# Kernel tuning notes

Measured on AMD Instinct MI355X. Metric: run time of the kernel, lower is better.

## Reference

```python
import jax, jax.numpy as jnp
import numpy as np

N, E = 50000, 800000          # nodes, edges
DC, EC, H, L = 128, 16, 64, 3 # data/edge channels, hidden, num GENConv layers
EPS_MSG = 1e-7                # GENConv message eps
LN_EPS = 1e-5                 # torch LayerNorm eps


def setup_inputs() -> dict:
    key = jax.random.key(0)
    ks = jax.random.split(key, 8)
    s = 0.05
    return {
        "x": jax.random.normal(ks[0], (N, DC), jnp.float32),
        "edge_index": jax.random.randint(ks[1], (2, E), 0, N),
        "edge_attr": jax.random.normal(ks[2], (E, EC), jnp.float32),
        # encoders
        "node_W": jax.random.normal(ks[3], (DC, H), jnp.float32) * s,
        "node_b": jnp.zeros((H,), jnp.float32),
        "edge_W": jax.random.normal(ks[4], (EC, H), jnp.float32) * s,
        "edge_b": jnp.zeros((H,), jnp.float32),
        # per-layer GENConv params (stacked over L layers)
        "t": jnp.ones((L,), jnp.float32),                       # learnable softmax temperature
        "mlp1_W": jax.random.normal(ks[5], (L, H, 2 * H), jnp.float32) * s,
        "mlp1_b": jnp.zeros((L, 2 * H), jnp.float32),
        "mlp_ln_g": jnp.ones((L, 2 * H), jnp.float32),
        "mlp_ln_b": jnp.zeros((L, 2 * H), jnp.float32),
        "mlp2_W": jax.random.normal(ks[6], (L, 2 * H, H), jnp.float32) * s,
        "mlp2_b": jnp.zeros((L, H), jnp.float32),
        # DeepGCNLayer res+ pre-norm params (index 0 also used as the final norm)
        "blk_ln_g": jnp.ones((L, H), jnp.float32),
        "blk_ln_b": jnp.zeros((L, H), jnp.float32),
    }


def _layernorm(h, g, b):
    mu = jnp.mean(h, axis=-1, keepdims=True)
    var = jnp.var(h, axis=-1, keepdims=True)
    return (h - mu) * jax.lax.rsqrt(var + LN_EPS) * g + b


def _genconv(h, src, dst, eattr, t, W1, b1, lng, lnb, W2, b2):
    # message: relu(x_j + edge_attr) + eps   -> [E, H]
    msg = jax.nn.relu(h[src] + eattr) + EPS_MSG
    # softmax aggregation over incoming edges of each dst node (per feature)
    s = msg * t
    smax = jax.ops.segment_max(s, dst, num_segments=N)
    e = jnp.exp(s - smax[dst])
    denom = jax.ops.segment_sum(e, dst, num_segments=N)
    w = e / denom[dst]
    agg = jax.ops.segment_sum(msg * w, dst, num_segments=N)
    out = agg + h  # root (x_r) residual inside GENConv
    # MLP: Linear(H,2H) -> LayerNorm -> ReLU -> Linear(2H,H)
    y = jax.nn.relu(_layernorm(out @ W1 + b1, lng, lnb))
    return y @ W2 + b2


def reference(x, edge_index, edge_attr, node_W, node_b, edge_W, edge_b, t,
              mlp1_W, mlp1_b, mlp_ln_g, mlp_ln_b, mlp2_W, mlp2_b,
              blk_ln_g, blk_ln_b):
    src, dst = edge_index[0], edge_index[1]
    h = x @ node_W + node_b
    ea = edge_attr @ edge_W + edge_b
    # layer 0: conv only (no pre-norm), as in DeeperGCN.forward
    h = _genconv(h, src, dst, ea, t[0], mlp1_W[0], mlp1_b[0],
                 mlp_ln_g[0], mlp_ln_b[0], mlp2_W[0], mlp2_b[0])
    # layers 1..L-1: res+ blocks (norm -> relu -> conv -> residual); dropout=0 in eval
    for i in range(1, L):
        z = jax.nn.relu(_layernorm(h, blk_ln_g[i], blk_ln_b[i]))
        h = h + _genconv(z, src, dst, ea, t[i], mlp1_W[i], mlp1_b[i],
                         mlp_ln_g[i], mlp_ln_b[i], mlp2_W[i], mlp2_b[i])
    # final: layers[0].norm + relu (dropout identity in eval)
    return jax.nn.relu(_layernorm(h, blk_ln_g[0], blk_ln_b[0]))
```

## Files before the change

kernel.cpp:

```cpp
#include <hip/hip_runtime.h>
#include <hip/hip_bf16.h>


#define LN_EPS 1e-5f
#define EPS_MSG 1e-7f

#define PF_NODEB 0
#define PF_EB    64
#define PF_T     128
#define PF_B1    132
#define PF_B2    516
#define PF_LNG   708
#define PF_LNB   1092
#define PF_BG    1476
#define PF_BB    1668
#define PF_TOT   1860
#define PW_NODEWT 0
#define PW_W1T    8192
#define PW_W2T    32768
#define PW_EW     57344
#define PW_EWT    58368
#define PW_TOT    59392

typedef __attribute__((ext_vector_type(8))) __bf16 bf16x8;
typedef __attribute__((ext_vector_type(4))) float floatx4;
typedef __attribute__((ext_vector_type(8))) unsigned short ushort8;

union FragU { bf16x8 v; ushort8 w; unsigned short u[8]; };

__device__ __forceinline__ float b2f(unsigned short u) {
    union { unsigned int i; float f; } v; v.i = ((unsigned int)u) << 16; return v.f;
}
__device__ __forceinline__ unsigned short f2b(float f) {
    unsigned int x = __builtin_bit_cast(unsigned int, f);
    x += 0x7fffu + ((x >> 16) & 1u);
    return (unsigned short)(x >> 16);
}
__device__ __forceinline__ float ldv(const void* p, size_t i, int f32) {
    return f32 ? ((const float*)p)[i] : b2f(((const unsigned short*)p)[i]);
}
__device__ __forceinline__ bf16x8 ld8(const void* p, size_t i, int f32) {
    FragU r;
    if (f32) {
        const float* fp = (const float*)p + i;
        floatx4 a = *(const floatx4*)fp;
        floatx4 b = *(const floatx4*)(fp + 4);
#pragma unroll
        for (int j = 0; j < 4; j++) { r.u[j] = f2b(a[j]); r.u[4 + j] = f2b(b[j]); }
    } else {
        r.w = *(const ushort8*)((const unsigned short*)p + i);
    }
    return r.v;
}
__device__ __forceinline__ int sniff(const void* tptr) {
    return ((const unsigned int*)tptr)[0] == 0x3F800000u ? 1 : 0;
}

__global__ __launch_bounds__(256) void k_wprep(
    const void* __restrict__ nodeW, const void* __restrict__ nodeB,
    const void* __restrict__ eW, const void* __restrict__ eb,
    const void* __restrict__ tp, const void* __restrict__ W1,
    const void* __restrict__ b1, const void* __restrict__ lng,
    const void* __restrict__ lnb, const void* __restrict__ W2,
    const void* __restrict__ b2, const void* __restrict__ bg,
    const void* __restrict__ bbp,
    float* __restrict__ pf, unsigned short* __restrict__ pw,
    int* __restrict__ counts, int N) {
    int f32 = sniff(tp);
    int gid = blockIdx.x * 256 + threadIdx.x;
    if (gid < N) counts[gid] = 0;
    if (gid < 8192) {
        int n = gid >> 7, k = gid & 127;
        pw[gid] = f2b(ldv(nodeW, (size_t)k * 64 + n, f32));
    } else if (gid < 32768) {
        int j = gid - 8192; int i = j >> 13; int r = j & 8191;
        int n = r >> 6, k = r & 63;
        pw[gid] = f2b(ldv(W1, (size_t)i * 8192 + (size_t)k * 128 + n, f32));
    } else if (gid < 57344) {
        int j = gid - 32768; int i = j >> 13; int r = j & 8191;
        int n = r >> 7, k = r & 127;
        pw[gid] = f2b(ldv(W2, (size_t)i * 8192 + (size_t)k * 64 + n, f32));
    } else if (gid < PW_EWT) {
        pw[gid] = f2b(ldv(eW, gid - PW_EW, f32));
    } else if (gid < PW_TOT) {
        int j = gid - PW_EWT; int n = j >> 4, k = j & 15;
        pw[gid] = f2b(ldv(eW, (size_t)k * 64 + n, f32));
    }
    if (gid < PF_TOT) {
        float v; int t = gid;
        if      (t < 64)   v = ldv(nodeB, t, f32);
        else if (t < 128)  v = ldv(eb, t - 64, f32);
        else if (t < 132)  v = (t - 128 < 3) ? ldv(tp, t - 128, f32) : 0.f;
        else if (t < 516)  v = ldv(b1, t - PF_B1, f32);
        else if (t < 708)  v = ldv(b2, t - PF_B2, f32);
        else if (t < 1092) v = ldv(lng, t - PF_LNG, f32);
        else if (t < 1476) v = ldv(lnb, t - PF_LNB, f32);
        else if (t < 1668) v = ldv(bg, t - PF_BG, f32);
        else               v = ldv(bbp, t - PF_BB, f32);
        pf[t] = v;
    }
}

__global__ __launch_bounds__(256) void k_hist_enc(const int* __restrict__ dst,
                                                  int* __restrict__ counts, int E,
                                                  int hist_blocks,
                                                  const void* __restrict__ x,
                                                  const unsigned short* __restrict__ pw,
                                                  const float* __restrict__ pf,
                                                  unsigned short* __restrict__ zb,
                                                  int N, const void* __restrict__ tptr) {
    if ((int)blockIdx.x < hist_blocks) {
        int i = blockIdx.x * 256 + threadIdx.x;
        if (i < E) atomicAdd(&counts[dst[i]], 1);
        return;
    }
    int f32 = sniff(tptr);
    int bid = blockIdx.x - hist_blocks;
    int wave = threadIdx.x >> 6, lane = threadIdx.x & 63;
    int tm = bid * 4 + wave;
    if (tm >= (N >> 4)) return;
    int l15 = lane & 15, quad = lane >> 4;
    int arow = tm * 16 + l15;
    floatx4 acc[4] = {{0,0,0,0},{0,0,0,0},{0,0,0,0},{0,0,0,0}};
#pragma unroll
    for (int kb = 0; kb < 4; kb++) {
        bf16x8 a = ld8(x, (size_t)arow * 128 + kb * 32 + quad * 8, f32);
#pragma unroll
        for (int tn = 0; tn < 4; tn++) {
            FragU b;
            b.w = *(const ushort8*)(pw + PW_NODEWT + (size_t)(tn * 16 + l15) * 128 + kb * 32 + quad * 8);
            acc[tn] = __builtin_amdgcn_mfma_f32_16x16x32_bf16(a, b.v, acc[tn], 0, 0, 0);
        }
    }
#pragma unroll
    for (int tn = 0; tn < 4; tn++) {
        int col = tn * 16 + l15;
        float bv = pf[PF_NODEB + col];
#pragma unroll
        for (int r = 0; r < 4; r++) {
            int row = tm * 16 + quad * 4 + r;
            zb[(size_t)row * 64 + col] = f2b(acc[tn][r] + bv);
        }
    }
}

__global__ __launch_bounds__(256) void k_scan1(const int* __restrict__ counts,
                                               int* __restrict__ bsum, int N) {
    __shared__ int ws[4];
    int tid = threadIdx.x, lane = tid & 63, w = tid >> 6;
    int i0 = blockIdx.x * 1024 + tid * 4;
    int s = 0;
#pragma unroll
    for (int k = 0; k < 4; k++) s += (i0 + k < N) ? counts[i0 + k] : 0;
#pragma unroll
    for (int m = 1; m < 64; m <<= 1) s += __shfl_xor(s, m);
    if (lane == 0) ws[w] = s;
    __syncthreads();
    if (tid == 0) bsum[blockIdx.x] = ws[0] + ws[1] + ws[2] + ws[3];
}

__global__ __launch_bounds__(1024) void k_scan2(const int* __restrict__ bsum,
                                                int* __restrict__ boff, int nb,
                                                int* __restrict__ row_startN) {
    __shared__ int wsum[16];
    int tid = threadIdx.x, lane = tid & 63, w = tid >> 6;
    int v = (tid < nb) ? bsum[tid] : 0;
    int incl = v;
#pragma unroll
    for (int m = 1; m < 64; m <<= 1) { int t = __shfl_up(incl, m); if (lane >= m) incl += t; }
    if (lane == 63) wsum[w] = incl;
    __syncthreads();
    if (w == 0) {
        int s = (lane < 16) ? wsum[lane] : 0;
#pragma unroll
        for (int m = 1; m < 16; m <<= 1) { int t = __shfl_up(s, m); if (lane >= m) s += t; }
        if (lane < 16) wsum[lane] = s;
    }
    __syncthreads();
    int woff = (w > 0) ? wsum[w - 1] : 0;
    if (tid < nb) boff[tid] = woff + incl - v;
    if (tid == nb - 1) row_startN[0] = woff + incl;
}

__global__ __launch_bounds__(256) void k_scan3(const int* __restrict__ counts,
                                               const int* __restrict__ boff,
                                               int* __restrict__ row_start,
                                               int* __restrict__ cursor, int N) {
    __shared__ int ws[4];
    int tid = threadIdx.x, lane = tid & 63, w = tid >> 6;
    int i0 = blockIdx.x * 1024 + tid * 4;
    int v[4];
#pragma unroll
    for (int k = 0; k < 4; k++) v[k] = (i0 + k < N) ? counts[i0 + k] : 0;
    int tsum = v[0] + v[1] + v[2] + v[3];
    int incl = tsum;
#pragma unroll
    for (int m = 1; m < 64; m <<= 1) { int t = __shfl_up(incl, m); if (lane >= m) incl += t; }
    if (lane == 63) ws[w] = incl;
    __syncthreads();
    int woff = 0;
    if (w > 0) woff += ws[0];
    if (w > 1) woff += ws[1];
    if (w > 2) woff += ws[2];
    int run = boff[blockIdx.x] + woff + incl - tsum;
#pragma unroll
    for (int k = 0; k < 4; k++) {
        if (i0 + k < N) { row_start[i0 + k] = run; cursor[i0 + k] = run; }
        run += v[k];
    }
}

__global__ __launch_bounds__(256) void k_perm(const int* __restrict__ dst,
                                              const int* __restrict__ src,
                                              int* __restrict__ cursor,
                                              int2* __restrict__ sortp, int E) {
    int e = blockIdx.x * blockDim.x + threadIdx.x;
    if (e < E) {
        int pos = atomicAdd(&cursor[dst[e]], 1);
        sortp[pos] = make_int2(e, src[e]);
    }
}

__global__ __launch_bounds__(256) void k_ea3(const void* __restrict__ eattr,
                                             const int2* __restrict__ sortp,
                                             const unsigned short* __restrict__ pw,
                                             const float* __restrict__ pf,
                                             unsigned short* __restrict__ ea_s,
                                             int E, const void* __restrict__ tptr) {
    __shared__ unsigned short lds[4 * 1088];
    int f32 = sniff(tptr);
    int wave = threadIdx.x >> 6, lane = threadIdx.x & 63;
    int p0 = (blockIdx.x * 4 + wave) * 16;
    if (p0 >= E) return;
    int l15 = lane & 15, quad = lane >> 4;
    unsigned short* L = lds + wave * 1088;
    FragU a;
#pragma unroll
    for (int j = 0; j < 8; j++) a.u[j] = 0;
    if (quad < 2) {
        int p = p0 + l15; if (p >= E) p = E - 1;
        int e = sortp[p].x;
        a.v = ld8(eattr, (size_t)e * 16 + quad * 8, f32);
    }
    floatx4 acc[4] = {{0,0,0,0},{0,0,0,0},{0,0,0,0},{0,0,0,0}};
#pragma unroll
    for (int tn = 0; tn < 4; tn++) {
        FragU b;
#pragma unroll
        for (int j = 0; j < 8; j++) b.u[j] = 0;
        if (quad < 2)
            b.w = *(const ushort8*)(pw + PW_EWT + (size_t)(tn * 16 + l15) * 16 + quad * 8);
        acc[tn] = __builtin_amdgcn_mfma_f32_16x16x32_bf16(a.v, b.v, acc[tn], 0, 0, 0);
    }
#pragma unroll
    for (int tn = 0; tn < 4; tn++) {
        int col = tn * 16 + l15;
        float bv = pf[PF_EB + col];
#pragma unroll
        for (int r = 0; r < 4; r++)
            L[(quad * 4 + r) * 68 + col] = f2b(acc[tn][r] + bv);
    }
    __builtin_amdgcn_s_waitcnt(0);
#pragma unroll
    for (int s = 0; s < 2; s++) {
        int row = (lane >> 3) + s * 8;
        int chunk = lane & 7;
        int grow = p0 + row;
        if (grow < E)
            *(ushort8*)(ea_s + (size_t)grow * 64 + chunk * 8) =
                *(const ushort8*)(L + row * 68 + chunk * 8);
    }
}

__global__ __launch_bounds__(256) void k_copy(const void* __restrict__ eattr,
                                              const int2* __restrict__ sortp,
                                              unsigned short* __restrict__ eattr_s,
                                              int E, const void* __restrict__ tptr) {
    int f32 = sniff(tptr);
    int gid = blockIdx.x * blockDim.x + threadIdx.x;
    int p = gid >> 4;
    int ch = gid & 15;
    if (p >= E) return;
    int e = sortp[p].x;
    float v = ldv(eattr, (size_t)e * 16 + ch, f32);
    eattr_s[(size_t)p * 16 + ch] = f2b(v);
}

__global__ __launch_bounds__(256) void k_edge_seg(const unsigned short* __restrict__ z,
                                                  const int2* __restrict__ sortp,
                                                  const int* __restrict__ row_start,
                                                  const unsigned short* __restrict__ eabuf,
                                                  const float* __restrict__ pf,
                                                  const unsigned short* __restrict__ pw,
                                                  int layer,
                                                  unsigned short* __restrict__ aggz,
                                                  int N, int stream_mode) {
    int wid = (blockIdx.x * blockDim.x + threadIdx.x) >> 6;
    int lane = threadIdx.x & 63;
    if (wid >= N) return;
    float t = pf[PF_T + layer];
    int s0 = row_start[wid], s1 = row_start[wid + 1];
    float num = 0.f, den = 0.f;
    if (stream_mode) {
        int j = s0;
        for (; j + 4 <= s1; j += 4) {
            int sa = sortp[j].y;
            int sb = sortp[j + 1].y;
            int sc = sortp[j + 2].y;
            int sd = sortp[j + 3].y;
            float za = b2f(z[(size_t)sa * 64 + lane]);
            float zb_ = b2f(z[(size_t)sb * 64 + lane]);
            float zc = b2f(z[(size_t)sc * 64 + lane]);
            float zd = b2f(z[(size_t)sd * 64 + lane]);
            float ea = b2f(eabuf[(size_t)j * 64 + lane]);
            float eb = b2f(eabuf[(size_t)(j + 1) * 64 + lane]);
            float ec = b2f(eabuf[(size_t)(j + 2) * 64 + lane]);
            float ed = b2f(eabuf[(size_t)(j + 3) * 64 + lane]);
            float m0 = fmaxf(za + ea, 0.f) + EPS_MSG;
            float m1 = fmaxf(zb_ + eb, 0.f) + EPS_MSG;
            float m2 = fmaxf(zc + ec, 0.f) + EPS_MSG;
            float m3 = fmaxf(zd + ed, 0.f) + EPS_MSG;
            float x0 = __expf(m0 * t);
            float x1 = __expf(m1 * t);
            float x2 = __expf(m2 * t);
            float x3 = __expf(m3 * t);
            num += m0 * x0 + m1 * x1 + m2 * x2 + m3 * x3;
            den += x0 + x1 + x2 + x3;
        }
        for (; j < s1; ++j) {
            int s = sortp[j].y;
            float zv = b2f(z[(size_t)s * 64 + lane]);
            float eav = b2f(eabuf[(size_t)j * 64 + lane]);
            float msg = fmaxf(zv + eav, 0.f) + EPS_MSG;
            float ex = __expf(msg * t);
            num += msg * ex;
            den += ex;
        }
    } else {
        float ew[16];
#pragma unroll
        for (int k = 0; k < 16; k++) ew[k] = b2f(pw[PW_EW + k * 64 + lane]);
        float ebv = pf[PF_EB + lane];
        for (int j = s0; j < s1; ++j) {
            int s = sortp[j].y;
            float zv = b2f(z[(size_t)s * 64 + lane]);
            const unsigned short* ap = eabuf + (size_t)j * 16;
            ushort8 a0 = *(const ushort8*)ap;
            ushort8 a1 = *(const ushort8*)(ap + 8);
            float ea = ebv;
#pragma unroll
            for (int k = 0; k < 8; k++) ea += ew[k] * b2f(a0[k]);
#pragma unroll
            for (int k = 0; k < 8; k++) ea += ew[8 + k] * b2f(a1[k]);
            float msg = fmaxf(zv + ea, 0.f) + EPS_MSG;
            float ex = __expf(msg * t);
            num += msg * ex;
            den += ex;
        }
    }
    float agg = (den > 0.f) ? __fdividef(num, den) : 0.f;
    float root = b2f(z[(size_t)wid * 64 + lane]);
    aggz[(size_t)wid * 64 + lane] = f2b(agg + root);
}

__global__ __launch_bounds__(256) void k_mlp(const unsigned short* __restrict__ aggz,
                                             const unsigned short* __restrict__ pw,
                                             const float* __restrict__ pf,
                                             int layer, float* __restrict__ h,
                                             void* __restrict__ zout,
                                             int N, int res, int last, int zidx,
                                             const void* __restrict__ tptr) {
    __shared__ unsigned short lds[4 * 2176];
    int wave = threadIdx.x >> 6, lane = threadIdx.x & 63;
    int tm = blockIdx.x * 4 + wave;
    if (tm >= (N >> 4)) return;
    int l15 = lane & 15, quad = lane >> 4;
    unsigned short* L = lds + wave * 2176;

    const unsigned short* W1T = pw + PW_W1T + (size_t)layer * 8192;
    int arow = tm * 16 + l15;
    FragU a0, a1;
    a0.w = *(const ushort8*)(aggz + (size_t)arow * 64 + quad * 8);
    a1.w = *(const ushort8*)(aggz + (size_t)arow * 64 + 32 + quad * 8);
    floatx4 acc1[8];
#pragma unroll
    for (int tn = 0; tn < 8; tn++) {
        FragU b0, b1;
        b0.w = *(const ushort8*)(W1T + (size_t)(tn * 16 + l15) * 64 + quad * 8);
        b1.w = *(const ushort8*)(W1T + (size_t)(tn * 16 + l15) * 64 + 32 + quad * 8);
        floatx4 z4 = {0.f, 0.f, 0.f, 0.f};
        z4 = __builtin_amdgcn_mfma_f32_16x16x32_bf16(a0.v, b0.v, z4, 0, 0, 0);
        acc1[tn] = __builtin_amdgcn_mfma_f32_16x16x32_bf16(a1.v, b1.v, z4, 0, 0, 0);
    }
    float s[4] = {0, 0, 0, 0}, q[4] = {0, 0, 0, 0};
#pragma unroll
    for (int tn = 0; tn < 8; tn++) {
        float bv = pf[PF_B1 + layer * 128 + tn * 16 + l15];
#pragma unroll
        for (int r = 0; r < 4; r++) {
            float v = acc1[tn][r] + bv;
            acc1[tn][r] = v;
            s[r] += v; q[r] += v * v;
        }
    }
    float mean[4], rs[4];
#pragma unroll
    for (int r = 0; r < 4; r++) {
        float sr = s[r], qr = q[r];
#pragma unroll
        for (int m = 1; m < 16; m <<= 1) { sr += __shfl_xor(sr, m); qr += __shfl_xor(qr, m); }
        mean[r] = sr * (1.f / 128.f);
        float var = qr * (1.f / 128.f) - mean[r] * mean[r];
        rs[r] = rsqrtf(var + LN_EPS);
    }
#pragma unroll
    for (int tn = 0; tn < 8; tn++) {
        int col = tn * 16 + l15;
        float g = pf[PF_LNG + layer * 128 + col];
        float bb = pf[PF_LNB + layer * 128 + col];
#pragma unroll
        for (int r = 0; r < 4; r++) {
            float y = fmaxf((acc1[tn][r] - mean[r]) * rs[r] * g + bb, 0.f);
            L[(quad * 4 + r) * 136 + col] = f2b(y);
        }
    }
    __builtin_amdgcn_s_waitcnt(0);

    const unsigned short* W2T = pw + PW_W2T + (size_t)layer * 8192;
    floatx4 acc2[4] = {{0,0,0,0},{0,0,0,0},{0,0,0,0},{0,0,0,0}};
#pragma unroll
    for (int kb = 0; kb < 4; kb++) {
        FragU a;
        a.w = *(const ushort8*)(L + l15 * 136 + kb * 32 + quad * 8);
#pragma unroll
        for (int tn = 0; tn < 4; tn++) {
            FragU b;
            b.w = *(const ushort8*)(W2T + (size_t)(tn * 16 + l15) * 128 + kb * 32 + quad * 8);
            acc2[tn] = __builtin_amdgcn_mfma_f32_16x16x32_bf16(a.v, b.v, acc2[tn], 0, 0, 0);
        }
    }
    float v[4][4];
    float s2[4] = {0, 0, 0, 0}, q2[4] = {0, 0, 0, 0};
#pragma unroll
    for (int tn = 0; tn < 4; tn++) {
        int col = tn * 16 + l15;
        float bv = pf[PF_B2 + layer * 64 + col];
#pragma unroll
        for (int r = 0; r < 4; r++) {
            int row = tm * 16 + quad * 4 + r;
            float t = acc2[tn][r] + bv;
            if (res) t += h[(size_t)row * 64 + col];
            if (!last) h[(size_t)row * 64 + col] = t;
            v[tn][r] = t;
            s2[r] += t; q2[r] += t * t;
        }
    }
    float mean2[4], rs2[4];
#pragma unroll
    for (int r = 0; r < 4; r++) {
        float sr = s2[r], qr = q2[r];
#pragma unroll
        for (int m = 1; m < 16; m <<= 1) { sr += __shfl_xor(sr, m); qr += __shfl_xor(qr, m); }
        mean2[r] = sr * (1.f / 64.f);
        float var = qr * (1.f / 64.f) - mean2[r] * mean2[r];
        rs2[r] = rsqrtf(var + LN_EPS);
    }
    int f32o = last ? sniff(tptr) : 0;
#pragma unroll
    for (int tn = 0; tn < 4; tn++) {
        int col = tn * 16 + l15;
        float g = pf[PF_BG + zidx * 64 + col];
        float bb = pf[PF_BB + zidx * 64 + col];
#pragma unroll
        for (int r = 0; r < 4; r++) {
            int row = tm * 16 + quad * 4 + r;
            float zv = fmaxf((v[tn][r] - mean2[r]) * rs2[r] * g + bb, 0.f);
            if (f32o) ((float*)zout)[(size_t)row * 64 + col] = zv;
            else      ((unsigned short*)zout)[(size_t)row * 64 + col] = f2b(zv);
        }
    }
}

extern "C" void kernel_launch(void* const* d_in, const int* in_sizes, int n_in,
                              void* d_out, int out_size, void* d_ws, size_t ws_size,
                              hipStream_t stream) {
    const void* x     = d_in[0];
    const int*  ei    = (const int*)d_in[1];
    const void* eattr = d_in[2];
    const void* nodeW = d_in[3];
    const void* nodeB = d_in[4];
    const void* edgeW = d_in[5];
    const void* edgeB = d_in[6];
    const void* tptr  = d_in[7];
    const void* W1    = d_in[8];
    const void* b1    = d_in[9];
    const void* lng   = d_in[10];
    const void* lnb   = d_in[11];
    const void* W2    = d_in[12];
    const void* b2    = d_in[13];
    const void* bg    = d_in[14];
    const void* bbp   = d_in[15];

    const int N = in_sizes[0] / 128;
    const int E = in_sizes[1] / 2;
    const int* srcp = ei;
    const int* dstp = ei + E;

    auto align256 = [](char* q) { return (char*)(((size_t)q + 255) & ~(size_t)255); };
    char* p = (char*)d_ws;
    float* h   = (float*)p;                    p = align256(p + (size_t)N * 64 * 4);
    unsigned short* zb   = (unsigned short*)p; p = align256(p + (size_t)N * 64 * 2);
    unsigned short* aggz = (unsigned short*)p; p = align256(p + (size_t)N * 64 * 2);
    int* counts     = (int*)p;                 p = align256(p + (size_t)N * 4);
    int* row_start  = (int*)p;                 p = align256(p + (size_t)(N + 1) * 4);
    int* cursor     = (int*)p;                 p = align256(p + (size_t)N * 4);
    int nsb = (N + 1023) / 1024;
    int* bsum       = (int*)p;                 p = align256(p + (size_t)nsb * 4);
    int* boff       = (int*)p;                 p = align256(p + (size_t)nsb * 4);
    int2* sortp     = (int2*)p;                p = align256(p + (size_t)E * 8);
    float* pf = (float*)p;                     p = align256(p + (size_t)PF_TOT * 4);
    unsigned short* pw = (unsigned short*)p;   p = align256(p + (size_t)PW_TOT * 2);
    unsigned short* edata = (unsigned short*)p;
    size_t base = (size_t)(p - (char*)d_ws);
    int stream_mode = (ws_size >= base + (size_t)E * 64 * 2) ? 1 : 0;

    auto blocks = [](long waves) { return dim3((unsigned)((waves * 64 + 255) / 256)); };
    int ntm_blocks = (N / 16 + 3) / 4;
    int wprep_blocks = ((N > PW_TOT ? N : PW_TOT) + 255) / 256;
    int hist_blocks = (E + 255) / 256;

    k_wprep<<<dim3(wprep_blocks), 256, 0, stream>>>(
        nodeW, nodeB, edgeW, edgeB, tptr, W1, b1, lng, lnb, W2, b2, bg, bbp,
        pf, pw, counts, N);

    k_hist_enc<<<dim3(hist_blocks + ntm_blocks), 256, 0, stream>>>(
        dstp, counts, E, hist_blocks, x, pw, pf, zb, N, tptr);

    k_scan1<<<dim3(nsb), 256, 0, stream>>>(counts, bsum, N);
    k_scan2<<<dim3(1), 1024, 0, stream>>>(bsum, boff, nsb, row_start + N);
    k_scan3<<<dim3(nsb), 256, 0, stream>>>(counts, boff, row_start, cursor, N);

    k_perm<<<dim3((E + 255) / 256), 256, 0, stream>>>(dstp, srcp, cursor, sortp, E);
    if (stream_mode)
        k_ea3<<<dim3(((E + 15) / 16 + 3) / 4), 256, 0, stream>>>(
            eattr, sortp, pw, pf, edata, E, tptr);
    else
        k_copy<<<dim3((E * 16 + 255) / 256), 256, 0, stream>>>(eattr, sortp,
                                                               edata, E, tptr);

    for (int i = 0; i < 3; i++) {
        k_edge_seg<<<blocks(N), 256, 0, stream>>>(zb, sortp, row_start, edata,
                                                  pf, pw, i, aggz, N, stream_mode);
        int last = (i == 2);
        k_mlp<<<dim3(ntm_blocks), 256, 0, stream>>>(
            aggz, pw, pf, i, h, last ? d_out : (void*)zb, N,
            i > 0 ? 1 : 0, last, last ? 0 : (i + 1), tptr);
    }
}
```

Before: 462.9 us.

## Record per-edge rank in histogram pass to drop atomics from permutation

```diff
diff --git a/kernel.cpp b/kernel.cpp
--- a/kernel.cpp
+++ b/kernel.cpp
@@ -102,7 +102,8 @@
 }
 
 __global__ __launch_bounds__(256) void k_hist_enc(const int* __restrict__ dst,
-                                                  int* __restrict__ counts, int E,
+                                                  int* __restrict__ counts,
+                                                  int* __restrict__ rank, int E,
                                                   int hist_blocks,
                                                   const void* __restrict__ x,
                                                   const unsigned short* __restrict__ pw,
@@ -110,8 +111,17 @@
                                                   unsigned short* __restrict__ zb,
                                                   int N, const void* __restrict__ tptr) {
     if ((int)blockIdx.x < hist_blocks) {
-        int i = blockIdx.x * 256 + threadIdx.x;
-        if (i < E) atomicAdd(&counts[dst[i]], 1);
+        int i0 = (blockIdx.x * 256 + threadIdx.x) * 4;
+        if (i0 + 4 <= E) {
+            int4 d4 = *(const int4*)(dst + i0);
+            int r0 = atomicAdd(&counts[d4.x], 1);
+            int r1 = atomicAdd(&counts[d4.y], 1);
+            int r2 = atomicAdd(&counts[d4.z], 1);
+            int r3 = atomicAdd(&counts[d4.w], 1);
+            *(int4*)(rank + i0) = make_int4(r0, r1, r2, r3);
+        } else {
+            for (int i = i0; i < E; i++) rank[i] = atomicAdd(&counts[dst[i]], 1);
+        }
         return;
     }
     int f32 = sniff(tptr);
@@ -184,8 +194,7 @@
 
 __global__ __launch_bounds__(256) void k_scan3(const int* __restrict__ counts,
                                                const int* __restrict__ boff,
-                                               int* __restrict__ row_start,
-                                               int* __restrict__ cursor, int N) {
+                                               int* __restrict__ row_start, int N) {
     __shared__ int ws[4];
     int tid = threadIdx.x, lane = tid & 63, w = tid >> 6;
     int i0 = blockIdx.x * 1024 + tid * 4;
@@ -205,19 +214,32 @@
     int run = boff[blockIdx.x] + woff + incl - tsum;
 #pragma unroll
     for (int k = 0; k < 4; k++) {
-        if (i0 + k < N) { row_start[i0 + k] = run; cursor[i0 + k] = run; }
+        if (i0 + k < N) row_start[i0 + k] = run;
         run += v[k];
     }
 }
 
 __global__ __launch_bounds__(256) void k_perm(const int* __restrict__ dst,
                                               const int* __restrict__ src,
-                                              int* __restrict__ cursor,
+                                              const int* __restrict__ rank,
+                                              const int* __restrict__ row_start,
                                               int2* __restrict__ sortp, int E) {
-    int e = blockIdx.x * blockDim.x + threadIdx.x;
-    if (e < E) {
-        int pos = atomicAdd(&cursor[dst[e]], 1);
-        sortp[pos] = make_int2(e, src[e]);
+    int e0 = (blockIdx.x * 256 + threadIdx.x) * 4;
+    if (e0 + 4 <= E) {
+        int4 d4 = *(const int4*)(dst + e0);
+        int4 r4 = *(const int4*)(rank + e0);
+        int4 s4 = *(const int4*)(src + e0);
+        int p0 = row_start[d4.x] + r4.x;
+        int p1 = row_start[d4.y] + r4.y;
+        int p2 = row_start[d4.z] + r4.z;
+        int p3 = row_start[d4.w] + r4.w;
+        sortp[p0] = make_int2(e0, s4.x);
+        sortp[p1] = make_int2(e0 + 1, s4.y);
+        sortp[p2] = make_int2(e0 + 2, s4.z);
+        sortp[p3] = make_int2(e0 + 3, s4.w);
+    } else {
+        for (int e = e0; e < E; e++)
+            sortp[row_start[dst[e]] + rank[e]] = make_int2(e, src[e]);
     }
 }
 
@@ -513,7 +535,7 @@
     unsigned short* aggz = (unsigned short*)p; p = align256(p + (size_t)N * 64 * 2);
     int* counts     = (int*)p;                 p = align256(p + (size_t)N * 4);
     int* row_start  = (int*)p;                 p = align256(p + (size_t)(N + 1) * 4);
-    int* cursor     = (int*)p;                 p = align256(p + (size_t)N * 4);
+    int* rank       = (int*)p;                 p = align256(p + (size_t)E * 4);
     int nsb = (N + 1023) / 1024;
     int* bsum       = (int*)p;                 p = align256(p + (size_t)nsb * 4);
     int* boff       = (int*)p;                 p = align256(p + (size_t)nsb * 4);
@@ -527,20 +549,21 @@
     auto blocks = [](long waves) { return dim3((unsigned)((waves * 64 + 255) / 256)); };
     int ntm_blocks = (N / 16 + 3) / 4;
     int wprep_blocks = ((N > PW_TOT ? N : PW_TOT) + 255) / 256;
-    int hist_blocks = (E + 255) / 256;
+    int hist_blocks = (E + 1023) / 1024;
 
     k_wprep<<<dim3(wprep_blocks), 256, 0, stream>>>(
         nodeW, nodeB, edgeW, edgeB, tptr, W1, b1, lng, lnb, W2, b2, bg, bbp,
         pf, pw, counts, N);
 
     k_hist_enc<<<dim3(hist_blocks + ntm_blocks), 256, 0, stream>>>(
-        dstp, counts, E, hist_blocks, x, pw, pf, zb, N, tptr);
+        dstp, counts, rank, E, hist_blocks, x, pw, pf, zb, N, tptr);
 
     k_scan1<<<dim3(nsb), 256, 0, stream>>>(counts, bsum, N);
     k_scan2<<<dim3(1), 1024, 0, stream>>>(bsum, boff, nsb, row_start + N);
-    k_scan3<<<dim3(nsb), 256, 0, stream>>>(counts, boff, row_start, cursor, N);
-
-    k_perm<<<dim3((E + 255) / 256), 256, 0, stream>>>(dstp, srcp, cursor, sortp, E);
+    k_scan3<<<dim3(nsb), 256, 0, stream>>>(counts, boff, row_start, N);
+
+    k_perm<<<dim3((E + 1023) / 1024), 256, 0, stream>>>(dstp, srcp, rank,
+                                                        row_start, sortp, E);
     if (stream_mode)
         k_ea3<<<dim3(((E + 15) / 16 + 3) / 4), 256, 0, stream>>>(
             eattr, sortp, pw, pf, edata, E, tptr);
```

New measurement: 433.6 us. 6.3% less time.
